# Optimization experiments

Measured on AMD Instinct MI355X. Metric: run time of the kernel, lower is better.

## Reference

```python
import jax, jax.numpy as jnp
import numpy as np

EGO, RNN, CUBE, FC, NA = 3200, 512, 3200, 1024, 2
N = 2048


def setup_inputs() -> dict:
    key = jax.random.key(0)
    ks = jax.random.split(key, 24)
    s = 0.02
    inp = {
        'rnn_feats': jax.random.normal(ks[0], (N, 2, RNN), jnp.float32),
        'cube_feats': jax.random.normal(ks[1], (N, 2, 4, CUBE), jnp.float32),
        'ego_feats': jax.random.normal(ks[2], (N, 3, EGO + RNN), jnp.float32),
        'rnn_eid': jax.random.randint(ks[3], (N,), 0, 3),
        'room_eid': jax.random.randint(ks[4], (N,), 0, 2),
        'dist_eid': jax.random.randint(ks[5], (N,), 0, 2),
        # shared front-end layers
        'Wc': jax.random.normal(ks[6], (CUBE, FC), jnp.float32) * s,
        'bc': jnp.zeros((FC,), jnp.float32),
        'Wd': jax.random.normal(ks[7], (EGO + RNN, FC), jnp.float32) * s,
        'bd': jnp.zeros((FC,), jnp.float32),
        # 3 experts on 2*RNN inputs (object color/size)
        'W1_rnn': jax.random.normal(ks[8], (3, 2 * RNN, FC), jnp.float32) * s,
        'b1_rnn': jnp.zeros((3, FC), jnp.float32),
        'W2_rnn': jax.random.normal(ks[9], (3, FC, NA), jnp.float32) * s,
        'b2_rnn': jnp.zeros((3, NA), jnp.float32),
        # 2 experts on 2*4*FC inputs (room size)
        'W1_room': jax.random.normal(ks[10], (2, 8 * FC, FC), jnp.float32) * s,
        'b1_room': jnp.zeros((2, FC), jnp.float32),
        'W2_room': jax.random.normal(ks[11], (2, FC, NA), jnp.float32) * s,
        'b2_room': jnp.zeros((2, NA), jnp.float32),
        # 2 experts on 2*FC inputs (object dist)
        'W1_dist': jax.random.normal(ks[12], (2, 2 * FC, FC), jnp.float32) * s,
        'b1_dist': jnp.zeros((2, FC), jnp.float32),
        'W2_dist': jax.random.normal(ks[13], (2, FC, NA), jnp.float32) * s,
        'b2_dist': jnp.zeros((2, NA), jnp.float32),
    }
    return inp


def _group_mlp(x, W1, b1, W2, b2, eid):
    # x: (n, in); W1: (E, in, fc); per-sample routed 2-layer MLP.
    # Dropout is identity (eval / p=0). Compute all E experts (E<=3), select via one-hot.
    h = jax.nn.relu(jnp.einsum('ni,eif->nef', x, W1) + b1[None])  # (n, E, fc)
    s = jnp.einsum('nef,efo->neo', h, W2) + b2[None]              # (n, E, 2)
    oh = jax.nn.one_hot(eid, W1.shape[0], dtype=x.dtype)          # (n, E)
    return jnp.einsum('neo,ne->no', s, oh)


def reference(rnn_feats, cube_feats, ego_feats, Wc, bc, Wd, bd,
              W1_rnn, b1_rnn, W2_rnn, b2_rnn,
              W1_room, b1_room, W2_room, b2_room,
              W1_dist, b1_dist, W2_dist, b2_dist,
              rnn_eid, room_eid, dist_eid):
    n = rnn_feats.shape[0]
    # object color/size group: raw rnn feats flattened
    x_rnn = rnn_feats.reshape(n, -1)                                   # (n, 2*RNN)
    s_rnn = _group_mlp(x_rnn, W1_rnn, b1_rnn, W2_rnn, b2_rnn, rnn_eid)
    # room size group: cube_fc_layer then flatten (2,4,fc) -> 8*fc
    hc = jax.nn.relu(jnp.einsum('npqc,cf->npqf', cube_feats, Wc) + bc)
    x_room = hc.reshape(n, -1)                                          # (n, 8*FC)
    s_room = _group_mlp(x_room, W1_room, b1_room, W2_room, b2_room, room_eid)
    # object dist group: dist_fc_layer, then pairwise products of the 3 rows
    hd = jax.nn.relu(jnp.einsum('nkd,df->nkf', ego_feats, Wd) + bd)     # (n, 3, FC)
    x_dist = jnp.concatenate([hd[:, 0] * hd[:, 1], hd[:, 1] * hd[:, 2]], axis=-1)  # (n, 2*FC)
    s_dist = _group_mlp(x_dist, W1_dist, b1_dist, W2_dist, b2_dist, dist_eid)
    return jnp.concatenate([s_rnn, s_room, s_dist], axis=0)             # (3n, 2)
```

## Files before the change

kernel.cpp:

```cpp
#include <hip/hip_runtime.h>

typedef __bf16 bf16;
typedef __bf16 bf16x8 __attribute__((ext_vector_type(8)));
typedef float f32x4 __attribute__((ext_vector_type(4)));

__device__ __forceinline__ void gld_lds16(const bf16* g, bf16* lds_base) {
    __builtin_amdgcn_global_load_lds(
        (const __attribute__((address_space(1))) void*)g,
        (__attribute__((address_space(3))) void*)lds_base, 16, 0, 0);
}

__global__ void detect_k(const unsigned* __restrict__ rnn, int* __restrict__ flag) {
    const int lane = threadIdx.x;
    const unsigned w = rnn[lane];
    const int e = (w >> 7) & 0xFF;
    const bool good = (e >= 100 && e <= 130);
    const unsigned long long m = __ballot(good);
    if (lane == 0) *flag = (__popcll(m) >= 48) ? 0 : 1;
}

__global__ __launch_bounds__(256) void transpose_k(const void* __restrict__ in_,
                                                   bf16* __restrict__ out,
                                                   const int* __restrict__ flag,
                                                   int R, int C) {
    __shared__ __align__(16) bf16 t[64][72];
    const int dt = *flag;
    const long boff = (long)blockIdx.z * R * C;
    const int c0 = blockIdx.x * 64, r0 = blockIdx.y * 64;
    const int lr = threadIdx.x >> 2;
    const int lc = (threadIdx.x & 3) * 16;

    bf16x8 v0, v1;
    if (dt) {
        const float* src = (const float*)in_ + boff + (long)(r0 + lr) * C + c0 + lc;
        float4 f0 = ((const float4*)src)[0];
        float4 f1 = ((const float4*)src)[1];
        float4 f2 = ((const float4*)src)[2];
        float4 f3 = ((const float4*)src)[3];
        v0[0]=(bf16)f0.x; v0[1]=(bf16)f0.y; v0[2]=(bf16)f0.z; v0[3]=(bf16)f0.w;
        v0[4]=(bf16)f1.x; v0[5]=(bf16)f1.y; v0[6]=(bf16)f1.z; v0[7]=(bf16)f1.w;
        v1[0]=(bf16)f2.x; v1[1]=(bf16)f2.y; v1[2]=(bf16)f2.z; v1[3]=(bf16)f2.w;
        v1[4]=(bf16)f3.x; v1[5]=(bf16)f3.y; v1[6]=(bf16)f3.z; v1[7]=(bf16)f3.w;
    } else {
        const bf16* src = (const bf16*)in_ + boff + (long)(r0 + lr) * C + c0 + lc;
        v0 = ((const bf16x8*)src)[0];
        v1 = ((const bf16x8*)src)[1];
    }
    *(bf16x8*)(&t[lr][lc])     = v0;
    *(bf16x8*)(&t[lr][lc + 8]) = v1;
    __syncthreads();

    bf16 tmp[16];
#pragma unroll
    for (int k = 0; k < 16; ++k) tmp[k] = t[lc + k][lr];
    bf16* dst = out + boff + (long)(c0 + lr) * R + r0 + lc;
    *(float4*)(dst)     = *(float4*)(&tmp[0]);
    *(float4*)(dst + 8) = *(float4*)(&tmp[8]);
}

__device__ __forceinline__ void mfma_tile(const bf16* As, const bf16* Bs,
                                          int wm, int wn, int quad, int l15,
                                          f32x4 acc[4][4]) {
#pragma unroll
    for (int kk = 0; kk < 2; ++kk) {
        bf16x8 af[4], bff[4];
        const int kc = kk * 4 + quad;
#pragma unroll
        for (int i = 0; i < 4; ++i) {
            const int m = wm * 64 + i * 16 + l15;
            af[i] = *(const bf16x8*)(As + m * 64 + (kc ^ (m & 7)) * 8);
            const int n = wn * 64 + i * 16 + l15;
            bff[i] = *(const bf16x8*)(Bs + n * 64 + (kc ^ (n & 7)) * 8);
        }
#pragma unroll
        for (int i = 0; i < 4; ++i)
#pragma unroll
            for (int j = 0; j < 4; ++j)
                acc[i][j] = __builtin_amdgcn_mfma_f32_16x16x32_bf16(
                    af[i], bff[j], acc[i][j], 0, 0, 0);
    }
}

__device__ __forceinline__ void stageAB(const bf16* a, const bf16* b, int K,
                                        bf16* Asb, bf16* Bsb, int lbase) {
#pragma unroll
    for (int r = 0; r < 4; ++r) {
        gld_lds16(a + (long)(r * 32) * K, Asb + r * 2048 + lbase);
        gld_lds16(b + (long)(r * 32) * K, Bsb + r * 2048 + lbase);
    }
}

__device__ __forceinline__ void stageB(const bf16* b, int K, bf16* Bsb, int lbase) {
#pragma unroll
    for (int r = 0; r < 4; ++r)
        gld_lds16(b + (long)(r * 32) * K, Bsb + r * 2048 + lbase);
}

__device__ __forceinline__ void issueA_f32(const char* Ag4, int K, int k0,
                                           float4 fa[8]) {
#pragma unroll
    for (int r = 0; r < 4; ++r) {
        const float4* pa = (const float4*)(Ag4 + ((long)(r * 32) * K + k0) * 4);
        fa[2 * r]     = pa[0];
        fa[2 * r + 1] = pa[1];
    }
}

__device__ __forceinline__ void writeA_cvt(bf16* Asb, const float4 fa[8], int ldst) {
#pragma unroll
    for (int r = 0; r < 4; ++r) {
        const float4 f0 = fa[2 * r], f1 = fa[2 * r + 1];
        bf16x8 v;
        v[0]=(bf16)f0.x; v[1]=(bf16)f0.y; v[2]=(bf16)f0.z; v[3]=(bf16)f0.w;
        v[4]=(bf16)f1.x; v[5]=(bf16)f1.y; v[6]=(bf16)f1.z; v[7]=(bf16)f1.w;
        *(bf16x8*)(Asb + r * 2048 + ldst) = v;
    }
}

__device__ __forceinline__ void kloop_bf16(const bf16* Agb, const bf16* Bg, int K,
                                           bf16* As, bf16* Bs, int lbase,
                                           int wm, int wn, int quad, int l15,
                                           f32x4 acc[4][4]) {
    const int nt = K >> 6;
    stageAB(Agb, Bg, K, As, Bs, lbase);
    for (int t = 0; t < nt; ++t) {
        const int cur = (t & 1) * 8192;
        if (t + 1 < nt) {
            const int nxt = ((t + 1) & 1) * 8192;
            stageAB(Agb + ((t + 1) << 6), Bg + ((t + 1) << 6), K,
                    As + nxt, Bs + nxt, lbase);
            asm volatile("s_waitcnt vmcnt(8)" ::: "memory");
        } else {
            asm volatile("s_waitcnt vmcnt(0)" ::: "memory");
        }
        __builtin_amdgcn_s_barrier();
        __builtin_amdgcn_sched_barrier(0);
        mfma_tile(As + cur, Bs + cur, wm, wn, quad, l15, acc);
        __builtin_amdgcn_sched_barrier(0);
        __builtin_amdgcn_s_barrier();
    }
}

__global__ __launch_bounds__(256, 2) void gemm_front(const void* __restrict__ A_,
                                                     const bf16* __restrict__ Bt,
                                                     const void* __restrict__ bias_,
                                                     bf16* __restrict__ C,
                                                     const int* __restrict__ flag,
                                                     int M, int N, int K) {
    __shared__ __align__(16) bf16 As[2][128 * 64];
    __shared__ __align__(16) bf16 Bs[2][128 * 64];

    const int dt = *flag;
    const int tid = threadIdx.x, lane = tid & 63, wid = tid >> 6;
    const int wm = wid & 1, wn = wid >> 1;

    const int lin = blockIdx.y * 8 + blockIdx.x;
    const int m0 = ((lin >> 6) * 8 + (lin & 7)) * 128;
    const int n0 = ((lin >> 3) & 7) * 128;

    const int srow = wid * 8 + (lane >> 3);
    const int scol = ((lane & 7) ^ (srow & 7)) * 8;
    const bf16* Bg = Bt + (long)(n0 + srow) * K + scol;
    const int ldst = wid * 512 + lane * 8;
    const int lbase = wid * 512;

    f32x4 acc[4][4];
#pragma unroll
    for (int i = 0; i < 4; ++i)
#pragma unroll
        for (int j = 0; j < 4; ++j) acc[i][j] = (f32x4){0.f, 0.f, 0.f, 0.f};

    const int quad = lane >> 4, l15 = lane & 15;
    const int nt = K >> 6;

    if (dt) {
        const char* Ag4 = (const char*)A_ + ((long)(m0 + srow) * K + scol) * 4;
        float4 fa[8];
        issueA_f32(Ag4, K, 0, fa);
        stageB(Bg, K, Bs[0], lbase);
        writeA_cvt(As[0], fa, ldst);
        __syncthreads();
        int t = 0;
        for (; t < nt - 2; t += 2) {
            issueA_f32(Ag4, K, (t + 1) << 6, fa);
            stageB(Bg + ((t + 1) << 6), K, Bs[1], lbase);
            mfma_tile(As[0], Bs[0], wm, wn, quad, l15, acc);
            writeA_cvt(As[1], fa, ldst);
            __syncthreads();
            issueA_f32(Ag4, K, (t + 2) << 6, fa);
            stageB(Bg + ((t + 2) << 6), K, Bs[0], lbase);
            mfma_tile(As[1], Bs[1], wm, wn, quad, l15, acc);
            writeA_cvt(As[0], fa, ldst);
            __syncthreads();
        }
        issueA_f32(Ag4, K, (nt - 1) << 6, fa);
        stageB(Bg + ((nt - 1) << 6), K, Bs[1], lbase);
        mfma_tile(As[0], Bs[0], wm, wn, quad, l15, acc);
        writeA_cvt(As[1], fa, ldst);
        __syncthreads();
        mfma_tile(As[1], Bs[1], wm, wn, quad, l15, acc);
    } else {
        const bf16* Agb = (const bf16*)A_ + (long)(m0 + srow) * K + scol;
        kloop_bf16(Agb, Bg, K, As[0], Bs[0], lbase, wm, wn, quad, l15, acc);
    }

#pragma unroll
    for (int j = 0; j < 4; ++j) {
        const int colg = n0 + wn * 64 + j * 16 + l15;
        const float bj = dt ? ((const float*)bias_)[colg]
                            : (float)((const bf16*)bias_)[colg];
#pragma unroll
        for (int i = 0; i < 4; ++i) {
            const int rowb = m0 + wm * 64 + i * 16 + quad * 4;
#pragma unroll
            for (int r = 0; r < 4; ++r) {
                float v = acc[i][j][r] + bj;
                v = v > 0.f ? v : 0.f;
                C[(long)(rowb + r) * N + colg] = (bf16)v;
            }
        }
    }
}

struct ExpDescs {
    const void* A[7];
    const bf16* Bt[7];
    const void* biasB[7];
    const void* w2B[7];
    float* S[7];
    long biasEoff[7];
    long w2Eoff[7];
    int K[7];
    int adt[7];
};

__global__ __launch_bounds__(256, 2) void gemm_expert(ExpDescs d,
                                                      const int* __restrict__ flag) {
    __shared__ __align__(16) bf16 As[2][128 * 64];
    __shared__ __align__(16) bf16 Bs[2][128 * 64];

    const int z = blockIdx.z;
    const int dt = *flag;
    const int adt = d.adt[z] ? dt : 0;
    const int K = d.K[z];
    const void* A_ = d.A[z];
    const bf16* Bt = d.Bt[z];

    const int tid = threadIdx.x, lane = tid & 63, wid = tid >> 6;
    const int wm = wid & 1, wn = wid >> 1;

    const int lin = blockIdx.y * 8 + blockIdx.x;
    const int m0 = ((lin >> 6) * 8 + (lin & 7)) * 128;
    const int n0 = ((lin >> 3) & 7) * 128;

    const int srow = wid * 8 + (lane >> 3);
    const int scol = ((lane & 7) ^ (srow & 7)) * 8;
    const bf16* Bg = Bt + (long)(n0 + srow) * K + scol;
    const int ldst = wid * 512 + lane * 8;
    const int lbase = wid * 512;

    f32x4 acc[4][4];
#pragma unroll
    for (int i = 0; i < 4; ++i)
#pragma unroll
        for (int j = 0; j < 4; ++j) acc[i][j] = (f32x4){0.f, 0.f, 0.f, 0.f};

    const int quad = lane >> 4, l15 = lane & 15;
    const int nt = K >> 6;

    if (adt) {
        const char* Ag4 = (const char*)A_ + ((long)(m0 + srow) * K + scol) * 4;
        float4 fa[8];
        issueA_f32(Ag4, K, 0, fa);
        stageB(Bg, K, Bs[0], lbase);
        writeA_cvt(As[0], fa, ldst);
        __syncthreads();
        int t = 0;
        for (; t < nt - 2; t += 2) {
            issueA_f32(Ag4, K, (t + 1) << 6, fa);
            stageB(Bg + ((t + 1) << 6), K, Bs[1], lbase);
            mfma_tile(As[0], Bs[0], wm, wn, quad, l15, acc);
            writeA_cvt(As[1], fa, ldst);
            __syncthreads();
            issueA_f32(Ag4, K, (t + 2) << 6, fa);
            stageB(Bg + ((t + 2) << 6), K, Bs[0], lbase);
            mfma_tile(As[1], Bs[1], wm, wn, quad, l15, acc);
            writeA_cvt(As[0], fa, ldst);
            __syncthreads();
        }
        issueA_f32(Ag4, K, (nt - 1) << 6, fa);
        stageB(Bg + ((nt - 1) << 6), K, Bs[1], lbase);
        mfma_tile(As[0], Bs[0], wm, wn, quad, l15, acc);
        writeA_cvt(As[1], fa, ldst);
        __syncthreads();
        mfma_tile(As[1], Bs[1], wm, wn, quad, l15, acc);
    } else {
        const bf16* Agb = (const bf16*)A_ + (long)(m0 + srow) * K + scol;
        kloop_bf16(Agb, Bg, K, As[0], Bs[0], lbase, wm, wn, quad, l15, acc);
    }

    const long besz = dt ? 4 : 2;
    const char* bias_b = (const char*)d.biasB[z] + d.biasEoff[z] * besz;
    const char* w2_b   = (const char*)d.w2B[z] + d.w2Eoff[z] * besz;
    float* S = d.S[z];

    float bj[4], w2f[4][2];
#pragma unroll
    for (int j = 0; j < 4; ++j) {
        const int colg = n0 + wn * 64 + j * 16 + l15;
        if (dt) {
            bj[j] = ((const float*)bias_b)[colg];
            w2f[j][0] = ((const float*)w2_b)[colg * 2 + 0];
            w2f[j][1] = ((const float*)w2_b)[colg * 2 + 1];
        } else {
            bj[j] = (float)((const bf16*)bias_b)[colg];
            w2f[j][0] = (float)((const bf16*)w2_b)[colg * 2 + 0];
            w2f[j][1] = (float)((const bf16*)w2_b)[colg * 2 + 1];
        }
    }
#pragma unroll
    for (int i = 0; i < 4; ++i) {
#pragma unroll
        for (int r = 0; r < 4; ++r) {
            float s0 = 0.f, s1 = 0.f;
#pragma unroll
            for (int j = 0; j < 4; ++j) {
                float h = acc[i][j][r] + bj[j];
                h = h > 0.f ? h : 0.f;
                s0 += h * w2f[j][0];
                s1 += h * w2f[j][1];
            }
#pragma unroll
            for (int msk = 1; msk < 16; msk <<= 1) {
                s0 += __shfl_xor(s0, msk);
                s1 += __shfl_xor(s1, msk);
            }
            if (l15 == 0) {
                const int rowg = m0 + wm * 64 + i * 16 + quad * 4 + r;
                atomicAdd(&S[rowg * 2 + 0], s0);
                atomicAdd(&S[rowg * 2 + 1], s1);
            }
        }
    }
}

__global__ __launch_bounds__(256) void pairprod_k(const bf16* __restrict__ hd,
                                                  bf16* __restrict__ xd) {
    const int idx = blockIdx.x * 256 + threadIdx.x;
    const int n = idx >> 8;
    const int c8 = (idx & 255) << 3;
    const bf16* p;
    if (c8 < 1024) p = hd + (long)(3 * n) * 1024 + c8;
    else           p = hd + (long)(3 * n + 1) * 1024 + (c8 - 1024);
    const bf16* q = p + 1024;
    bf16x8 a = *(const bf16x8*)p, b = *(const bf16x8*)q;
    bf16x8 o;
#pragma unroll
    for (int k = 0; k < 8; ++k) o[k] = (bf16)((float)a[k] * (float)b[k]);
    *(bf16x8*)(xd + (long)n * 2048 + c8) = o;
}

__global__ __launch_bounds__(256) void finalize_k(const float* __restrict__ S,
        const int* __restrict__ rnn_eid, const int* __restrict__ room_eid,
        const int* __restrict__ dist_eid, const void* __restrict__ b2_rnn,
        const void* __restrict__ b2_room, const void* __restrict__ b2_dist,
        const int* __restrict__ flag, void* __restrict__ out) {
    const int idx = blockIdx.x * 256 + threadIdx.x;
    if (idx >= 12288) return;
    const int dt = *flag;
    const int o = idx & 1;
    const int row = idx >> 1;
    const int g = row >> 11;
    const int n = row & 2047;
    float v;
    if (g == 0) {
        int e = rnn_eid[n]; e = e < 0 ? 0 : (e > 2 ? 2 : e);
        v = S[e * 4096 + n * 2 + o] +
            (dt ? ((const float*)b2_rnn)[e * 2 + o]
                : (float)((const bf16*)b2_rnn)[e * 2 + o]);
    } else if (g == 1) {
        int e = room_eid[n]; e = e < 0 ? 0 : (e > 1 ? 1 : e);
        v = S[12288 + e * 4096 + n * 2 + o] +
            (dt ? ((const float*)b2_room)[e * 2 + o]
                : (float)((const bf16*)b2_room)[e * 2 + o]);
    } else {
        int e = dist_eid[n]; e = e < 0 ? 0 : (e > 1 ? 1 : e);
        v = S[20480 + e * 4096 + n * 2 + o] +
            (dt ? ((const float*)b2_dist)[e * 2 + o]
                : (float)((const bf16*)b2_dist)[e * 2 + o]);
    }
    if (dt) ((float*)out)[idx] = v;
    else    ((bf16*)out)[idx] = (bf16)v;
}

extern "C" void kernel_launch(void* const* d_in, const int* in_sizes, int n_in,
                              void* d_out, int out_size, void* d_ws, size_t ws_size,
                              hipStream_t stream) {
    const void* rnn_feats = d_in[0];
    const void* cube      = d_in[1];
    const void* ego       = d_in[2];
    const int* rnn_eid    = (const int*)d_in[3];
    const int* room_eid   = (const int*)d_in[4];
    const int* dist_eid   = (const int*)d_in[5];
    const void* Wc        = d_in[6];
    const void* bc        = d_in[7];
    const void* Wd        = d_in[8];
    const void* bd        = d_in[9];
    const void* W1_rnn    = d_in[10];
    const void* b1_rnn    = d_in[11];
    const void* W2_rnn    = d_in[12];
    const void* b2_rnn    = d_in[13];
    const void* W1_room   = d_in[14];
    const void* b1_room   = d_in[15];
    const void* W2_room   = d_in[16];
    const void* b2_room   = d_in[17];
    const void* W1_dist   = d_in[18];
    const void* b1_dist   = d_in[19];
    const void* W2_dist   = d_in[20];
    const void* b2_dist   = d_in[21];

    char* ws = (char*)d_ws;
    float* S     = (float*)ws;
    int* flag    = (int*)(ws + 114688);
    bf16* WcT    = (bf16*)(ws + 114944);
    bf16* WdT    = (bf16*)(ws + 6668544);
    bf16* WrnnT  = (bf16*)(ws + 14270720);
    bf16* WroomT = (bf16*)(ws + 20562176);
    bf16* WdistT = (bf16*)(ws + 54116608);
    bf16* hc     = (bf16*)(ws + 62505216);
    bf16* hd     = (bf16*)(ws + 96059648);
    bf16* xd     = (bf16*)(ws + 108642560);

    detect_k<<<1, 64, 0, stream>>>((const unsigned*)rnn_feats, flag);
    hipMemsetAsync(S, 0, 114688, stream);

    transpose_k<<<dim3(16, 50, 1),  256, 0, stream>>>(Wc,      WcT,    flag, 3200, 1024);
    transpose_k<<<dim3(16, 58, 1),  256, 0, stream>>>(Wd,      WdT,    flag, 3712, 1024);
    transpose_k<<<dim3(16, 16, 3),  256, 0, stream>>>(W1_rnn,  WrnnT,  flag, 1024, 1024);
    transpose_k<<<dim3(16, 128, 2), 256, 0, stream>>>(W1_room, WroomT, flag, 8192, 1024);
    transpose_k<<<dim3(16, 32, 2),  256, 0, stream>>>(W1_dist, WdistT, flag, 2048, 1024);

    gemm_front<<<dim3(8, 128), 256, 0, stream>>>(cube, WcT, bc, hc, flag,
                                                 16384, 1024, 3200);
    gemm_front<<<dim3(8, 48), 256, 0, stream>>>(ego, WdT, bd, hd, flag,
                                                6144, 1024, 3712);
    pairprod_k<<<2048, 256, 0, stream>>>(hd, xd);

    ExpDescs D;
    for (int e = 0; e < 2; ++e) {
        const int z = e;
        D.A[z] = hc;                   D.Bt[z] = WroomT + (long)e * 1024 * 8192;
        D.biasB[z] = b1_room;          D.biasEoff[z] = (long)e * 1024;
        D.w2B[z] = W2_room;            D.w2Eoff[z] = (long)e * 2048;
        D.S[z] = S + 12288 + e * 4096; D.K[z] = 8192;  D.adt[z] = 0;
    }
    for (int e = 0; e < 2; ++e) {
        const int z = 2 + e;
        D.A[z] = xd;                   D.Bt[z] = WdistT + (long)e * 1024 * 2048;
        D.biasB[z] = b1_dist;          D.biasEoff[z] = (long)e * 1024;
        D.w2B[z] = W2_dist;            D.w2Eoff[z] = (long)e * 2048;
        D.S[z] = S + 20480 + e * 4096; D.K[z] = 2048;  D.adt[z] = 0;
    }
    for (int e = 0; e < 3; ++e) {
        const int z = 4 + e;
        D.A[z] = rnn_feats;            D.Bt[z] = WrnnT + (long)e * 1024 * 1024;
        D.biasB[z] = b1_rnn;           D.biasEoff[z] = (long)e * 1024;
        D.w2B[z] = W2_rnn;             D.w2Eoff[z] = (long)e * 2048;
        D.S[z] = S + e * 4096;         D.K[z] = 1024;  D.adt[z] = 1;
    }
    gemm_expert<<<dim3(8, 16, 7), 256, 0, stream>>>(D, flag);

    finalize_k<<<48, 256, 0, stream>>>(S, rnn_eid, room_eid, dist_eid,
                                       b2_rnn, b2_room, b2_dist, flag, d_out);
}
```

Baseline: 878.9 us.

## Add 256x256-tile 8-wave bf16 GEMM kernels with split-phase LDS pipelining

Adds 512-thread GEMM kernels with 256x256 output tiles for the front layers and the routed expert layers. They stream A and B through a 4-slot LDS ring using direct global-to-LDS loads and interleave four MFMA quadrants with prefetch, using s_setprio and barriers. The aim is more data reuse per tile and better overlap of loads with compute. These kernels run only when the runtime dtype flag says the inputs are bf16; the old 128-tile kernels now handle only the fp32 case. Each path launches both kernels and returns early on the wrong flag, which adds a few empty launches.

```diff
diff --git a/kernel.cpp b/kernel.cpp
--- a/kernel.cpp
+++ b/kernel.cpp
@@ -9,6 +9,8 @@
         (const __attribute__((address_space(1))) void*)g,
         (__attribute__((address_space(3))) void*)lds_base, 16, 0, 0);
 }
+
+#define MFMA16(a, b, c) __builtin_amdgcn_mfma_f32_16x16x32_bf16((a), (b), (c), 0, 0, 0)
 
 __global__ void detect_k(const unsigned* __restrict__ rnn, int* __restrict__ flag) {
     const int lane = threadIdx.x;
@@ -58,6 +60,286 @@
     *(float4*)(dst + 8) = *(float4*)(&tmp[8]);
 }
 
+__device__ __forceinline__ void kloop256(const bf16* __restrict__ A,
+                                         const bf16* __restrict__ Bt,
+                                         int K, int m0, int n0, bf16* L,
+                                         int wid, int lane,
+                                         f32x4 (&acc)[2][2][4][2]) {
+    const int wm = wid >> 2, wn = wid & 3;
+    const int quad = lane >> 4, l15 = lane & 15;
+    const int nt = K >> 6;
+
+    const int sr = wid * 8 + (lane >> 3);
+    const int sc = ((lane & 7) ^ ((lane >> 3) & 7)) * 8;
+    const bf16* Ag = A + (long)(m0 + sr) * K + sc;
+    const bf16* Bg = Bt + (long)(n0 + sr) * K + sc;
+    const long K64 = (long)K * 64, K128 = (long)K * 128;
+    bf16* const As = L;
+    bf16* const Bs = L + 32768;
+    const int w512 = wid * 512;
+
+    const int arow = (wm * 64 + l15) * 64;
+    const int brow = (wn * 32 + l15) * 64;
+    const int swz0 = ((0 * 4 + quad) ^ (l15 & 7)) * 8;
+    const int swz1 = ((1 * 4 + quad) ^ (l15 & 7)) * 8;
+
+    gld_lds16(Ag,              As + w512);
+    gld_lds16(Ag + K64,        As + 4096 + w512);
+    gld_lds16(Bg,              Bs + w512);
+    gld_lds16(Bg + K64,        Bs + 4096 + w512);
+    gld_lds16(Ag + K128,       As + 8192 + w512);
+    gld_lds16(Ag + K128 + K64, As + 8192 + 4096 + w512);
+    gld_lds16(Bg + K128,       Bs + 8192 + w512);
+    gld_lds16(Bg + K128 + K64, Bs + 8192 + 4096 + w512);
+    gld_lds16(Ag + 64,         As + 16384 + w512);
+    gld_lds16(Ag + K64 + 64,   As + 16384 + 4096 + w512);
+    gld_lds16(Bg + 64,         Bs + 16384 + w512);
+    gld_lds16(Bg + K64 + 64,   Bs + 16384 + 4096 + w512);
+    asm volatile("s_waitcnt vmcnt(4)" ::: "memory");
+    __builtin_amdgcn_s_barrier();
+
+    bf16x8 af[4][2], b0[2][2], b1[2][2];
+
+    for (int t = 0; t < nt; ++t) {
+        const int buf = t & 1, nbuf = buf ^ 1;
+        bf16* A0 = As + (buf * 2 + 0) * 8192;
+        bf16* A1 = As + (buf * 2 + 1) * 8192;
+        bf16* B0 = Bs + (buf * 2 + 0) * 8192;
+        bf16* B1 = Bs + (buf * 2 + 1) * 8192;
+        const long ko1 = (long)(t + 1) * 64;
+        const long ko2 = (long)(t + 2) * 64;
+
+#pragma unroll
+        for (int m = 0; m < 4; ++m) {
+            af[m][0] = *(const bf16x8*)(A0 + arow + m * 1024 + swz0);
+            af[m][1] = *(const bf16x8*)(A0 + arow + m * 1024 + swz1);
+        }
+#pragma unroll
+        for (int n = 0; n < 2; ++n) {
+            b0[n][0] = *(const bf16x8*)(B0 + brow + n * 1024 + swz0);
+            b0[n][1] = *(const bf16x8*)(B0 + brow + n * 1024 + swz1);
+        }
+        if (t + 1 < nt) {
+            gld_lds16(Ag + K128 + ko1,       As + (nbuf * 2 + 1) * 8192 + w512);
+            gld_lds16(Ag + K128 + K64 + ko1, As + (nbuf * 2 + 1) * 8192 + 4096 + w512);
+            gld_lds16(Bg + K128 + ko1,       Bs + (nbuf * 2 + 1) * 8192 + w512);
+            gld_lds16(Bg + K128 + K64 + ko1, Bs + (nbuf * 2 + 1) * 8192 + 4096 + w512);
+        }
+        __builtin_amdgcn_s_barrier();
+        asm volatile("s_waitcnt lgkmcnt(0)" ::: "memory");
+        __builtin_amdgcn_sched_barrier(0);
+        __builtin_amdgcn_s_setprio(1);
+#pragma unroll
+        for (int m = 0; m < 4; ++m)
+#pragma unroll
+            for (int n = 0; n < 2; ++n) {
+                acc[0][0][m][n] = MFMA16(af[m][0], b0[n][0], acc[0][0][m][n]);
+                acc[0][0][m][n] = MFMA16(af[m][1], b0[n][1], acc[0][0][m][n]);
+            }
+        __builtin_amdgcn_s_setprio(0);
+        __builtin_amdgcn_sched_barrier(0);
+        __builtin_amdgcn_s_barrier();
+
+#pragma unroll
+        for (int n = 0; n < 2; ++n) {
+            b1[n][0] = *(const bf16x8*)(B1 + brow + n * 1024 + swz0);
+            b1[n][1] = *(const bf16x8*)(B1 + brow + n * 1024 + swz1);
+        }
+        if (t + 2 < nt) {
+            gld_lds16(Ag + ko2,       A0 + w512);
+            gld_lds16(Ag + K64 + ko2, A0 + 4096 + w512);
+        }
+        __builtin_amdgcn_s_barrier();
+        asm volatile("s_waitcnt lgkmcnt(0)" ::: "memory");
+        __builtin_amdgcn_sched_barrier(0);
+        __builtin_amdgcn_s_setprio(1);
+#pragma unroll
+        for (int m = 0; m < 4; ++m)
+#pragma unroll
+            for (int n = 0; n < 2; ++n) {
+                acc[0][1][m][n] = MFMA16(af[m][0], b1[n][0], acc[0][1][m][n]);
+                acc[0][1][m][n] = MFMA16(af[m][1], b1[n][1], acc[0][1][m][n]);
+            }
+        __builtin_amdgcn_s_setprio(0);
+        __builtin_amdgcn_sched_barrier(0);
+        __builtin_amdgcn_s_barrier();
+
+#pragma unroll
+        for (int m = 0; m < 4; ++m) {
+            af[m][0] = *(const bf16x8*)(A1 + arow + m * 1024 + swz0);
+            af[m][1] = *(const bf16x8*)(A1 + arow + m * 1024 + swz1);
+        }
+        __builtin_amdgcn_s_barrier();
+        asm volatile("s_waitcnt lgkmcnt(0)" ::: "memory");
+        __builtin_amdgcn_sched_barrier(0);
+        __builtin_amdgcn_s_setprio(1);
+#pragma unroll
+        for (int m = 0; m < 4; ++m)
+#pragma unroll
+            for (int n = 0; n < 2; ++n) {
+                acc[1][0][m][n] = MFMA16(af[m][0], b0[n][0], acc[1][0][m][n]);
+                acc[1][0][m][n] = MFMA16(af[m][1], b0[n][1], acc[1][0][m][n]);
+            }
+        __builtin_amdgcn_s_setprio(0);
+        __builtin_amdgcn_sched_barrier(0);
+        __builtin_amdgcn_s_barrier();
+
+        if (t + 2 < nt) {
+            gld_lds16(Bg + ko2,       B0 + w512);
+            gld_lds16(Bg + K64 + ko2, B0 + 4096 + w512);
+        }
+        __builtin_amdgcn_s_setprio(1);
+#pragma unroll
+        for (int m = 0; m < 4; ++m)
+#pragma unroll
+            for (int n = 0; n < 2; ++n) {
+                acc[1][1][m][n] = MFMA16(af[m][0], b1[n][0], acc[1][1][m][n]);
+                acc[1][1][m][n] = MFMA16(af[m][1], b1[n][1], acc[1][1][m][n]);
+            }
+        __builtin_amdgcn_s_setprio(0);
+        __builtin_amdgcn_sched_barrier(0);
+        if (t + 2 < nt) {
+            asm volatile("s_waitcnt vmcnt(4)" ::: "memory");
+        } else if (t + 1 < nt) {
+            asm volatile("s_waitcnt vmcnt(0)" ::: "memory");
+        }
+        __builtin_amdgcn_s_barrier();
+    }
+}
+
+__device__ __forceinline__ void tile256_coords(int& m0, int& n0) {
+    const int lin = blockIdx.y * 8 + blockIdx.x;
+    const int x = lin & 7, j = lin >> 3;
+    const int mbPerX = (int)(gridDim.x * gridDim.y) >> 5;
+    m0 = (x * mbPerX + (j >> 2)) * 256;
+    n0 = (j & 3) * 256;
+}
+
+__global__ __launch_bounds__(512, 2) void gemm256_front(
+        const void* __restrict__ A_, const bf16* __restrict__ Bt,
+        const void* __restrict__ bias_, bf16* __restrict__ C,
+        const int* __restrict__ flag, int M, int N, int K) {
+    if (*flag != 0) return;
+    __shared__ __align__(16) bf16 L[65536];
+    const int tid = threadIdx.x, lane = tid & 63, wid = tid >> 6;
+    int m0, n0;
+    tile256_coords(m0, n0);
+
+    f32x4 acc[2][2][4][2];
+#pragma unroll
+    for (int a = 0; a < 2; ++a)
+#pragma unroll
+        for (int b = 0; b < 2; ++b)
+#pragma unroll
+            for (int m = 0; m < 4; ++m)
+#pragma unroll
+                for (int n = 0; n < 2; ++n) acc[a][b][m][n] = (f32x4){0.f,0.f,0.f,0.f};
+
+    kloop256((const bf16*)A_, Bt, K, m0, n0, L, wid, lane, acc);
+
+    const bf16* bias = (const bf16*)bias_;
+    const int wm = wid >> 2, wn = wid & 3;
+    const int quad = lane >> 4, l15 = lane & 15;
+#pragma unroll
+    for (int qn = 0; qn < 2; ++qn)
+#pragma unroll
+        for (int n = 0; n < 2; ++n) {
+            const int colg = n0 + qn * 128 + wn * 32 + n * 16 + l15;
+            const float bj = (float)bias[colg];
+#pragma unroll
+            for (int qm = 0; qm < 2; ++qm)
+#pragma unroll
+                for (int m = 0; m < 4; ++m) {
+                    const int rowb = m0 + qm * 128 + wm * 64 + m * 16 + quad * 4;
+#pragma unroll
+                    for (int r = 0; r < 4; ++r) {
+                        float v = acc[qm][qn][m][n][r] + bj;
+                        v = v > 0.f ? v : 0.f;
+                        C[(long)(rowb + r) * N + colg] = (bf16)v;
+                    }
+                }
+        }
+}
+
+struct ExpDescs {
+    const void* A[7];
+    const bf16* Bt[7];
+    const void* biasB[7];
+    const void* w2B[7];
+    float* S[7];
+    long biasEoff[7];
+    long w2Eoff[7];
+    int K[7];
+    int adt[7];
+};
+
+__global__ __launch_bounds__(512, 2) void gemm256_expert(ExpDescs d,
+                                                         const int* __restrict__ flag) {
+    if (*flag != 0) return;
+    __shared__ __align__(16) bf16 L[65536];
+    const int z = blockIdx.z;
+    const int K = d.K[z];
+    const int tid = threadIdx.x, lane = tid & 63, wid = tid >> 6;
+    int m0, n0;
+    tile256_coords(m0, n0);
+
+    f32x4 acc[2][2][4][2];
+#pragma unroll
+    for (int a = 0; a < 2; ++a)
+#pragma unroll
+        for (int b = 0; b < 2; ++b)
+#pragma unroll
+            for (int m = 0; m < 4; ++m)
+#pragma unroll
+                for (int n = 0; n < 2; ++n) acc[a][b][m][n] = (f32x4){0.f,0.f,0.f,0.f};
+
+    kloop256((const bf16*)d.A[z], d.Bt[z], K, m0, n0, L, wid, lane, acc);
+
+    const bf16* bias_b = (const bf16*)d.biasB[z] + d.biasEoff[z];
+    const bf16* w2_b   = (const bf16*)d.w2B[z] + d.w2Eoff[z];
+    float* S = d.S[z];
+    const int wm = wid >> 2, wn = wid & 3;
+    const int quad = lane >> 4, l15 = lane & 15;
+
+    float bj[2][2], w2f[2][2][2];
+#pragma unroll
+    for (int qn = 0; qn < 2; ++qn)
+#pragma unroll
+        for (int n = 0; n < 2; ++n) {
+            const int colg = n0 + qn * 128 + wn * 32 + n * 16 + l15;
+            bj[qn][n] = (float)bias_b[colg];
+            w2f[qn][n][0] = (float)w2_b[colg * 2 + 0];
+            w2f[qn][n][1] = (float)w2_b[colg * 2 + 1];
+        }
+#pragma unroll
+    for (int qm = 0; qm < 2; ++qm)
+#pragma unroll
+        for (int m = 0; m < 4; ++m)
+#pragma unroll
+            for (int r = 0; r < 4; ++r) {
+                float s0 = 0.f, s1 = 0.f;
+#pragma unroll
+                for (int qn = 0; qn < 2; ++qn)
+#pragma unroll
+                    for (int n = 0; n < 2; ++n) {
+                        float h = acc[qm][qn][m][n][r] + bj[qn][n];
+                        h = h > 0.f ? h : 0.f;
+                        s0 += h * w2f[qn][n][0];
+                        s1 += h * w2f[qn][n][1];
+                    }
+#pragma unroll
+                for (int msk = 1; msk < 16; msk <<= 1) {
+                    s0 += __shfl_xor(s0, msk);
+                    s1 += __shfl_xor(s1, msk);
+                }
+                if (l15 == 0) {
+                    const int rowg = m0 + qm * 128 + wm * 64 + m * 16 + quad * 4 + r;
+                    atomicAdd(&S[rowg * 2 + 0], s0);
+                    atomicAdd(&S[rowg * 2 + 1], s1);
+                }
+            }
+}
+
 __device__ __forceinline__ void mfma_tile(const bf16* As, const bf16* Bs,
                                           int wm, int wn, int quad, int l15,
                                           f32x4 acc[4][4]) {
@@ -147,10 +429,11 @@
                                                      bf16* __restrict__ C,
                                                      const int* __restrict__ flag,
                                                      int M, int N, int K) {
+    const int dt = *flag;
+    if (dt == 0) return;
     __shared__ __align__(16) bf16 As[2][128 * 64];
     __shared__ __align__(16) bf16 Bs[2][128 * 64];
 
-    const int dt = *flag;
     const int tid = threadIdx.x, lane = tid & 63, wid = tid >> 6;
     const int wm = wid & 1, wn = wid >> 1;
 
@@ -173,7 +456,7 @@
     const int quad = lane >> 4, l15 = lane & 15;
     const int nt = K >> 6;
 
-    if (dt) {
+    {
         const char* Ag4 = (const char*)A_ + ((long)(m0 + srow) * K + scol) * 4;
         float4 fa[8];
         issueA_f32(Ag4, K, 0, fa);
@@ -199,16 +482,12 @@
         writeA_cvt(As[1], fa, ldst);
         __syncthreads();
         mfma_tile(As[1], Bs[1], wm, wn, quad, l15, acc);
-    } else {
-        const bf16* Agb = (const bf16*)A_ + (long)(m0 + srow) * K + scol;
-        kloop_bf16(Agb, Bg, K, As[0], Bs[0], lbase, wm, wn, quad, l15, acc);
     }
 
 #pragma unroll
     for (int j = 0; j < 4; ++j) {
         const int colg = n0 + wn * 64 + j * 16 + l15;
-        const float bj = dt ? ((const float*)bias_)[colg]
-                            : (float)((const bf16*)bias_)[colg];
+        const float bj = ((const float*)bias_)[colg];
 #pragma unroll
         for (int i = 0; i < 4; ++i) {
             const int rowb = m0 + wm * 64 + i * 16 + quad * 4;
@@ -222,26 +501,15 @@
     }
 }
 
-struct ExpDescs {
-    const void* A[7];
-    const bf16* Bt[7];
-    const void* biasB[7];
-    const void* w2B[7];
-    float* S[7];
-    long biasEoff[7];
-    long w2Eoff[7];
-    int K[7];
-    int adt[7];
-};
-
 __global__ __launch_bounds__(256, 2) void gemm_expert(ExpDescs d,
                                                       const int* __restrict__ flag) {
+    const int dt = *flag;
+    if (dt == 0) return;
     __shared__ __align__(16) bf16 As[2][128 * 64];
     __shared__ __align__(16) bf16 Bs[2][128 * 64];
 
     const int z = blockIdx.z;
-    const int dt = *flag;
-    const int adt = d.adt[z] ? dt : 0;
+    const int adt = d.adt[z];
     const int K = d.K[z];
     const void* A_ = d.A[z];
     const bf16* Bt = d.Bt[z];
@@ -299,24 +567,17 @@
         kloop_bf16(Agb, Bg, K, As[0], Bs[0], lbase, wm, wn, quad, l15, acc);
     }
 
-    const long besz = dt ? 4 : 2;
-    const char* bias_b = (const char*)d.biasB[z] + d.biasEoff[z] * besz;
-    const char* w2_b   = (const char*)d.w2B[z] + d.w2Eoff[z] * besz;
+    const char* bias_b = (const char*)d.biasB[z] + d.biasEoff[z] * 4;
+    const char* w2_b   = (const char*)d.w2B[z] + d.w2Eoff[z] * 4;
     float* S = d.S[z];
 
     float bj[4], w2f[4][2];
 #pragma unroll
     for (int j = 0; j < 4; ++j) {
         const int colg = n0 + wn * 64 + j * 16 + l15;
-        if (dt) {
-            bj[j] = ((const float*)bias_b)[colg];
-            w2f[j][0] = ((const float*)w2_b)[colg * 2 + 0];
-            w2f[j][1] = ((const float*)w2_b)[colg * 2 + 1];
-        } else {
-            bj[j] = (float)((const bf16*)bias_b)[colg];
-            w2f[j][0] = (float)((const bf16*)w2_b)[colg * 2 + 0];
-            w2f[j][1] = (float)((const bf16*)w2_b)[colg * 2 + 1];
-        }
+        bj[j] = ((const float*)bias_b)[colg];
+        w2f[j][0] = ((const float*)w2_b)[colg * 2 + 0];
+        w2f[j][1] = ((const float*)w2_b)[colg * 2 + 1];
     }
 #pragma unroll
     for (int i = 0; i < 4; ++i) {
@@ -440,8 +701,12 @@
     transpose_k<<<dim3(16, 128, 2), 256, 0, stream>>>(W1_room, WroomT, flag, 8192, 1024);
     transpose_k<<<dim3(16, 32, 2),  256, 0, stream>>>(W1_dist, WdistT, flag, 2048, 1024);
 
+    gemm256_front<<<dim3(8, 32), 512, 0, stream>>>(cube, WcT, bc, hc, flag,
+                                                   16384, 1024, 3200);
     gemm_front<<<dim3(8, 128), 256, 0, stream>>>(cube, WcT, bc, hc, flag,
                                                  16384, 1024, 3200);
+    gemm256_front<<<dim3(8, 12), 512, 0, stream>>>(ego, WdT, bd, hd, flag,
+                                                   6144, 1024, 3712);
     gemm_front<<<dim3(8, 48), 256, 0, stream>>>(ego, WdT, bd, hd, flag,
                                                 6144, 1024, 3712);
     pairprod_k<<<2048, 256, 0, stream>>>(hd, xd);
@@ -468,6 +733,7 @@
         D.w2B[z] = W2_rnn;             D.w2Eoff[z] = (long)e * 2048;
         D.S[z] = S + e * 4096;         D.K[z] = 1024;  D.adt[z] = 1;
     }
+    gemm256_expert<<<dim3(8, 4, 7), 512, 0, stream>>>(D, flag);
     gemm_expert<<<dim3(8, 16, 7), 256, 0, stream>>>(D, flag);
 
     finalize_k<<<48, 256, 0, stream>>>(S, rnn_eid, room_eid, dist_eid,
```

Measured after the change: 958.0 us. 1.09x slower.
